# Performance work log

Hardware: AMD Instinct MI355X
Metric: run time of the kernel (lower is better)

## Reference

```python
import jax, jax.numpy as jnp
import numpy as np
from math import comb

N_DERIV = 4          # num_derivatives
ODE_DIM = 512        # ode_dimension
K = ODE_DIM * (N_DERIV + 1)


def _build_system(n, d):
    # system_matrices_1d: A_1d = flip(pascal), Q_1d = flip(hilbert), chol(Q_1d)
    x = np.arange(n + 1)
    B = np.array([[comb(i, j) for j in range(n + 1)] for i in range(n + 1)], dtype=np.float64)
    A1 = B[::-1, ::-1]                                  # flip both axes
    Hil = 1.0 / (x[:, None] + x[None, :] + 1.0)
    Q1 = Hil[::-1, ::-1]
    L1 = np.linalg.cholesky(Q1)
    a = np.kron(np.eye(d), A1)
    q = np.kron(np.eye(d), L1)
    return jnp.asarray(a, jnp.float32), jnp.asarray(q, jnp.float32)


def _qr_r(x):
    # sqrtm_to_cholesky: upper-triangular factor from reduced QR
    return jnp.linalg.qr(x)[1]


def setup_inputs() -> dict:
    key = jax.random.key(0)
    k1, k2, k3, k4, k5 = jax.random.split(key, 5)
    a, q_sqrtm_lower = _build_system(N_DERIV, ODE_DIM)
    m0 = jax.random.normal(k1, (K,), dtype=jnp.float32)
    l0 = jnp.tril(jax.random.normal(k2, (K, K), dtype=jnp.float32) * 0.05)
    H = jax.random.normal(k3, (ODE_DIM, K), dtype=jnp.float32) * 0.1
    bias = jax.random.normal(k4, (ODE_DIM,), dtype=jnp.float32)
    dt = jax.random.uniform(k5, (1,), dtype=jnp.float32, minval=0.05, maxval=0.15)
    return {"m0": m0, "l0": l0, "H": H, "bias": bias, "dt": dt,
            "a": a, "q_sqrtm_lower": q_sqrtm_lower}


def reference(m0, l0, H, bias, dt, a, q_sqrtm_lower):
    d = H.shape[0]
    k = m0.shape[0]
    n1 = k // d                       # num_derivatives + 1
    # --- assemble_preconditioner ---
    powers = jnp.arange(n1 - 1, -1, -1, dtype=m0.dtype)
    scales = jnp.exp(jax.lax.lgamma(powers + 1.0))
    pw = powers + 0.5
    adt = jnp.abs(dt[0])
    p = jnp.tile(adt ** pw / scales, d)          # (k,)
    p_inv = jnp.tile(adt ** (-pw) * scales, d)   # (k,)
    # --- extrapolate_mean ---
    m0_p = p_inv * m0
    m_ext_p = a @ m0_p
    m_ext = p * m_ext_p
    # EK-style linearized observation residual
    m_obs = H @ m_ext - bias                     # (d,)
    # --- estimate_error ---
    l_obs_ns_e = H @ (p_inv[:, None] * q_sqrtm_lower)            # (d,k)
    l_obs_raw = _qr_r(l_obs_ns_e.T).T                            # lower (d,d)
    res_white = jax.scipy.linalg.solve_triangular(l_obs_raw.T, m_obs, lower=False)
    diffusion = jnp.sqrt(jnp.dot(res_white, res_white) / res_white.size)
    error = diffusion * jnp.sqrt(jnp.einsum('nj,nj->n', l_obs_raw, l_obs_raw))
    # --- complete_extrapolation (sum_of_sqrtm_factors) ---
    R1 = (a @ (p_inv[:, None] * l0)).T           # (k,k)
    R2 = (diffusion * q_sqrtm_lower).T           # (k,k)
    l_ext_p = _qr_r(jnp.vstack([R1, R2])).T      # lower (k,k)
    l_ext = p[:, None] * l_ext_p
    # --- final_correction ---
    l_obs_ns = H @ l_ext                         # (d,k)
    l_obs = _qr_r(l_obs_ns.T).T                  # lower (d,d)
    crosscov = l_ext @ l_obs_ns.T                # (k,d)
    gain = jax.scipy.linalg.cho_solve((l_obs, True), crosscov.T).T  # (k,d)
    m_cor = m_ext - gain @ m_obs
    l_cor = l_ext - gain @ l_obs_ns
    u = jnp.reshape(m_cor, (-1, d), order='F')[0]  # derivative-0 block
    return m_cor, l_cor, u, error, diffusion
```

## Files before the change

kernel.cpp:

```cpp
#include <hip/hip_runtime.h>
#include <math.h>

#define KDIM 2560
#define DDIM 512
#define NB 64

#define QM 2560
#define QM2 1024
#define QN 512
#define PW 16
#define QACT 528

#define OUT_LCOR 2560
#define OUT_U    6556160
#define OUT_ERR  6556672
#define OUT_DIFF 6557184


__global__ void k_setup(const float* dt, double* scal){
  if (threadIdx.x==0 && blockIdx.x==0){
    double adt = fabs((double)dt[0]);
    const double scales[5] = {24.0,6.0,2.0,1.0,1.0};
    for (int i=0;i<5;i++){
      double pw = (double)(4-i)+0.5;
      scal[i]   = pow(adt, pw)/scales[i];
      scal[5+i] = pow(adt,-pw)*scales[i];
    }
  }
}

__global__ __launch_bounds__(256) void k_mext_mobs(const float* a, const float* m0, const float* H,
                                                   const float* bias, const double* scal,
                                                   double* mext, double* mobs){
  __shared__ double me[KDIM];
  __shared__ double red[256];
  double pp[5], pv[5];
  #pragma unroll
  for (int i=0;i<5;i++){ pp[i]=scal[i]; pv[i]=scal[5+i]; }
  int tid=threadIdx.x;
  for (int r=tid; r<KDIM; r+=256){
    int j=r/5, i=r%5;
    const float* arow = a + (size_t)r*KDIM + 5*j;
    const float* m0b  = m0 + 5*j;
    double acc=0;
    #pragma unroll
    for (int l=0;l<5;l++) acc += (double)arow[l]*pv[l]*(double)m0b[l];
    me[r] = pp[i]*acc;
  }
  __syncthreads();
  if (blockIdx.x==0) for (int r=tid;r<KDIM;r+=256) mext[r]=me[r];
  int b = blockIdx.x;
  const float* Hr = H + (size_t)b*KDIM;
  double acc=0;
  for (int c=tid;c<KDIM;c+=256) acc += (double)Hr[c]*me[c];
  red[tid]=acc; __syncthreads();
  for (int s=128;s>0;s>>=1){ if (tid<s) red[tid]+=red[tid+s]; __syncthreads(); }
  if (tid==0) mobs[b] = red[0] - (double)bias[b];
}

__global__ void k_A2(const float* H, const float* q, const double* scal,
                     double* Atop, double* Abot){
  int idx = blockIdx.x*blockDim.x+threadIdx.x;
  if (idx >= QN*QM) return;
  double pv[5];
  #pragma unroll
  for (int t=0;t<5;t++) pv[t]=scal[5+t];
  int j = idx / QM;
  int i = idx % QM;
  int bi = i/5;
  double acc=0;
  #pragma unroll
  for (int t=0;t<5;t++)
    acc += (double)H[(size_t)j*QM + 5*bi+t]*pv[t]*(double)q[(size_t)(5*bi+t)*QM + i];
  if (i < 512) Atop[(size_t)j*QM2 + i] = acc;
  else         Abot[(size_t)j*2048 + (i-512)] = acc;
}

__global__ void k_copyB(const double* Gbot, double* AQ){
  int idx = blockIdx.x*blockDim.x+threadIdx.x;
  if (idx >= 512*512) return;
  int c = idx/512, rr = idx%512;
  AQ[(size_t)c*QM2 + 512 + rr] = (rr<=c) ? Gbot[(size_t)c*512 + rr] : 0.0;
}

__global__ __launch_bounds__(576) void qr_step(double* A, double* vhead, double* Tbufs, int p){
  int col0 = p*PW;
  int tid=threadIdx.x, wid=tid>>6, lane=tid&63;

  if (blockIdx.x > 0){
    int pc0 = col0 - PW;
    const double* T = Tbufs + (size_t)(p-1)*PW*PW;
    int cc = col0 + PW + ((int)blockIdx.x - 1);
    int m = QM2 - pc0; if (m>QACT) m=QACT;
    __shared__ double redu[9][PW];
    __shared__ double yshu[PW];
    __shared__ double wshu[PW];
    int lr = tid;
    double a = (lr<m)? A[(size_t)cc*QM2 + pc0 + lr] : 0.0;
    double vv[PW];
    #pragma unroll
    for (int j=0;j<PW;j++){
      double vj=0.0;
      if (lr<m){
        if (lr>j)       vj=A[(size_t)(pc0+j)*QM2 + pc0 + lr];
        else if (lr==j) vj=vhead[pc0+j];
      }
      vv[j]=vj;
    }
    #pragma unroll
    for (int j=0;j<PW;j++){
      double d=vv[j]*a;
      #pragma unroll
      for (int o=32;o>0;o>>=1) d+=__shfl_down(d,o);
      if (lane==0) redu[wid][j]=d;
    }
    __syncthreads();
    if (tid<PW){
      double y=0;
      #pragma unroll
      for (int t=0;t<9;t++) y+=redu[t][tid];
      yshu[tid]=y;
    }
    __syncthreads();
    if (tid<PW){
      double s=0;
      for (int t=0;t<=tid;t++) s+=T[t*PW+tid]*yshu[t];
      wshu[tid]=s;
    }
    __syncthreads();
    if (lr<m){
      double s=0;
      #pragma unroll
      for (int j=0;j<PW;j++) s+=vv[j]*wshu[j];
      A[(size_t)cc*QM2 + pc0 + lr]=a-s;
    }
    return;
  }

  __shared__ double redw[9][PW];
  __shared__ double rednorm[9];
  __shared__ double sh[3];
  __shared__ double wsh[PW];
  __shared__ double alphas[PW], betas[PW];
  __shared__ double VtVs[PW][PW];
  __shared__ double Tsh[PW][PW];
  __shared__ double redP[9][PW*PW];
  __shared__ double ysh2[PW][PW];
  __shared__ double wsh2[PW][PW];

  int m = QM2 - col0; if (m>QACT) m=QACT;
  bool on = tid < m;
  double x[PW];

  if (p>0){
    int pc0 = col0 - PW;
    const double* T = Tbufs + (size_t)(p-1)*PW*PW;
    int mp = QM2 - pc0; if (mp>QACT) mp=QACT;
    bool gA = on;
    bool gB = (tid>=560);
    int rowA = col0 + tid;
    int kB   = tid - 560;
    double vv[PW];
    #pragma unroll
    for (int j=0;j<PW;j++){
      double vj=0.0;
      if (gA){
        if (tid + PW < mp) vj = A[(size_t)(pc0+j)*QM2 + rowA];
      } else if (gB){
        if (kB>j)       vj=A[(size_t)(pc0+j)*QM2 + pc0 + kB];
        else if (kB==j) vj=vhead[pc0+j];
      }
      vv[j]=vj;
    }
    #pragma unroll
    for (int c=0;c<PW;c++){
      double a=0.0;
      if (gA)      a = A[(size_t)(col0+c)*QM2 + rowA];
      else if (gB) a = A[(size_t)(col0+c)*QM2 + pc0 + kB];
      x[c]=a;
    }
    #pragma unroll
    for (int c=0;c<PW;c++){
      #pragma unroll
      for (int j=0;j<PW;j++){
        double d=vv[j]*x[c];
        #pragma unroll
        for (int o=32;o>0;o>>=1) d+=__shfl_down(d,o);
        if (lane==0) redP[wid][c*PW+j]=d;
      }
    }
    __syncthreads();
    if (tid<PW*PW){
      double y=0;
      #pragma unroll
      for (int t=0;t<9;t++) y+=redP[t][tid];
      ysh2[tid>>4][tid&15]=y;
    }
    __syncthreads();
    if (tid<PW*PW){
      int c=tid>>4, jj=tid&15;
      double s=0;
      for (int t=0;t<=jj;t++) s+=T[t*PW+jj]*ysh2[c][t];
      wsh2[c][jj]=s;
    }
    __syncthreads();
    #pragma unroll
    for (int c=0;c<PW;c++){
      double s=0;
      #pragma unroll
      for (int j=0;j<PW;j++) s+=vv[j]*wsh2[c][j];
      x[c]-=s;
    }
    if (gB){
      #pragma unroll
      for (int c=0;c<PW;c++) A[(size_t)(col0+c)*QM2 + pc0 + kB] = x[c];
    }
    if (!on){
      #pragma unroll
      for (int c=0;c<PW;c++) x[c]=0.0;
    }
    __syncthreads();
  } else {
    #pragma unroll
    for (int j=0;j<PW;j++)
      x[j] = on ? A[(size_t)(col0+j)*QM2 + col0 + tid] : 0.0;
  }

  #pragma unroll
  for (int j=0;j<PW;j++){
    double v0 = (tid>=j && on)? x[j] : 0.0;
    double ps = v0*v0;
    #pragma unroll
    for (int o=32;o>0;o>>=1) ps += __shfl_down(ps,o);
    if (lane==0) rednorm[wid]=ps;
    if (tid==j) sh[0]=x[j];
    __syncthreads();
    if (tid==0){
      double s0=0;
      for (int t=0;t<9;t++) s0+=rednorm[t];
      double x1=sh[0];
      double nrm=sqrt(s0);
      double alpha=(x1>=0.0)?-nrm:nrm;
      double v1=x1-alpha;
      double vtv=s0-2.0*alpha*x1+alpha*alpha;
      double b=(vtv>0.0)?2.0/vtv:0.0;
      sh[1]=v1; sh[2]=b;
      alphas[j]=alpha; betas[j]=b;
      vhead[col0+j]=v1;
    }
    __syncthreads();
    if (tid==j) x[j]=sh[1];
    double b=sh[2];
    double v=(tid>=j && on)? x[j] : 0.0;
    #pragma unroll
    for (int t=0;t<PW;t++){
      if (t==j) continue;
      double pdot=v*x[t];
      #pragma unroll
      for (int o=32;o>0;o>>=1) pdot+=__shfl_down(pdot,o);
      if (lane==0) redw[wid][t]=pdot;
    }
    __syncthreads();
    if (tid<PW && tid!=j){
      double tot=0;
      #pragma unroll
      for (int t2=0;t2<9;t2++) tot+=redw[t2][tid];
      if (tid>j) wsh[tid]=b*tot;
      else       VtVs[tid][j]=tot;
    }
    __syncthreads();
    if (v!=0.0){
      #pragma unroll
      for (int t=j+1;t<PW;t++) x[t]-=wsh[t]*v;
    }
  }
  __syncthreads();
  if (tid<PW){
    int i=tid;
    Tsh[i][i]=betas[i];
    for (int j2=i+1;j2<PW;j2++){
      double z=0;
      for (int t=i;t<j2;t++) z+=Tsh[i][t]*VtVs[t][j2];
      Tsh[i][j2]=-betas[j2]*z;
    }
  }
  __syncthreads();
  for (int e=tid;e<PW*PW;e+=576){
    int i=e/PW, j2=e%PW;
    Tbufs[(size_t)p*PW*PW + e] = (j2>=i)? Tsh[i][j2] : 0.0;
  }
  if (on){
    #pragma unroll
    for (int j=0;j<PW;j++)
      A[(size_t)(col0+j)*QM2 + col0 + tid] = (tid==j)? alphas[j] : x[j];
  }
}

__global__ __launch_bounds__(512) void k_rpost(const double* Aq, const double* mobs,
                                               double* scal, float* out){
  __shared__ double b[DDIM];
  __shared__ double xs[DDIM];
  __shared__ double D[NB][NB+1];
  __shared__ double red[DDIM];
  __shared__ double g1sh[DDIM];
  int tid=threadIdx.x;
  {
    double s=0;
    for (int r=0;r<=tid;r++){ double v=Aq[(size_t)tid*QM2 + r]; s+=v*v; }
    g1sh[tid]=s;
  }
  b[tid]=mobs[tid];
  __syncthreads();
  for (int p=7;p>=0;p--){
    int b0=p*NB;
    for (int e=tid;e<NB*NB;e+=512){ int i=e&63, j2=e>>6; D[i][j2]=Aq[(size_t)(b0+j2)*QM2 + b0+i]; }
    __syncthreads();
    if (tid<64){
      double bi=b[b0+tid];
      for (int k=NB-1;k>=0;k--){
        double bk=__shfl(bi,k);
        double xk=bk/D[k][k];
        if (tid<k) bi-=D[tid][k]*xk;
        if (tid==k) bi=xk;
      }
      xs[b0+tid]=bi;
    }
    __syncthreads();
    if (tid<b0){
      double s=0;
      #pragma unroll 8
      for (int j2=0;j2<NB;j2++) s+=Aq[(size_t)(b0+j2)*QM2 + tid]*xs[b0+j2];
      b[tid]-=s;
    }
    __syncthreads();
  }
  red[tid]=xs[tid]*xs[tid]; __syncthreads();
  for (int s=256;s>0;s>>=1){ if (tid<s) red[tid]+=red[tid+s]; __syncthreads(); }
  double diff=sqrt(red[0]/(double)DDIM);
  if (tid==0){ scal[10]=diff; out[OUT_DIFF]=(float)diff; }
  out[OUT_ERR+tid]=(float)(diff*sqrt(fmax(g1sh[tid],0.0)));
}

__global__ void k_X(const float* a, const float* l0, const double* scal, float* X){
  int idx=blockIdx.x*blockDim.x+threadIdx.x;
  if (idx>=KDIM*KDIM) return;
  double pv[5];
  #pragma unroll
  for (int t=0;t<5;t++) pv[t]=scal[5+t];
  int r=idx/KDIM, c=idx%KDIM;
  int j=r/5;
  const float* arow = a + (size_t)r*KDIM + 5*j;
  double acc=0;
  #pragma unroll
  for (int l=0;l<5;l++)
    acc += (double)arow[l]*pv[l]*(double)l0[(size_t)(5*j+l)*KDIM+c];
  X[idx]=(float)acc;
}

template<typename TA,int ATR,typename TB,int BTR,int MODE>
__global__ __launch_bounds__(256) void gemm32(const TA* __restrict__ A,int lda,
                                              const TB* __restrict__ B,int ldb,
                                              void* __restrict__ Cv,int ldc,
                                              int K,int kmode){
  __shared__ double As[32][33];
  __shared__ double Bs[32][33];
  int tid=threadIdx.x, tx=tid&15, ty=tid>>4;
  int n0=blockIdx.x*32, m0=blockIdx.y*32;
  int ks=0, ke=K;
  if (kmode==1) ks=n0;
  else if (kmode==2) ke=min(K,n0+32);
  else if (kmode==3) ke=min(K,m0+32);
  else if (kmode==4) ks=m0;
  double acc[2][2]={};
  for (int k0=ks;k0<ke;k0+=32){
    if (ATR){
      for (int e=tid;e<32*32;e+=256){int k=e>>5,mm=e&31; As[k][mm]=(double)A[(size_t)(k0+k)*lda+m0+mm];}
    } else {
      for (int e=tid;e<32*32;e+=256){int mm=e>>5,k=e&31; As[k][mm]=(double)A[(size_t)(m0+mm)*lda+k0+k];}
    }
    if (BTR){
      for (int e=tid;e<32*32;e+=256){int nn=e>>5,k=e&31; Bs[k][nn]=(double)B[(size_t)(n0+nn)*ldb+k0+k];}
    } else {
      for (int e=tid;e<32*32;e+=256){int k=e>>5,nn=e&31; Bs[k][nn]=(double)B[(size_t)(k0+k)*ldb+n0+nn];}
    }
    __syncthreads();
    #pragma unroll
    for (int t=0;t<32;t++){
      double av[2],bv[2];
      #pragma unroll
      for (int i=0;i<2;i++){av[i]=As[t][ty+16*i];bv[i]=Bs[t][tx+16*i];}
      #pragma unroll
      for (int i=0;i<2;i++)
        #pragma unroll
        for (int j=0;j<2;j++) acc[i][j]+=av[i]*bv[j];
    }
    __syncthreads();
  }
  #pragma unroll
  for (int i=0;i<2;i++){
    #pragma unroll
    for (int j=0;j<2;j++){
      size_t idx=(size_t)(m0+ty+16*i)*ldc+n0+tx+16*j;
      if (MODE==0) ((double*)Cv)[idx]=acc[i][j];
      else if (MODE==1) ((double*)Cv)[idx]-=acc[i][j];
      else ((float*)Cv)[idx]=(float)acc[i][j];
    }
  }
}

__global__ __launch_bounds__(256) void syrk_lower(const float* __restrict__ X, const float* __restrict__ q,
                                                  const double* __restrict__ scal,
                                                  double* __restrict__ G, int n){
  int t = blockIdx.x;
  int u = (int)((sqrtf(8.0f*(float)t+1.0f)+1.0f)*0.5f);
  while ((u*(u-1))/2 > t) u--;
  while ((u*(u+1))/2 <= t) u++;
  int s = (KDIM/64) - u;
  int r = s + (t - (u*(u-1))/2);
  int S0=s*64, R0=r*64;
  __shared__ double As[16][65];
  __shared__ double Bs[16][65];
  int tid=threadIdx.x, tx=tid&15, ty=tid>>4;
  int kend=min(n, S0+80);
  double acc[4][4]={};
  for (int k0=0;k0<kend;k0+=16){
    for (int e=tid;e<64*16;e+=256){int mm=e>>4,k=e&15; As[k][mm]=(double)X[(size_t)(R0+mm)*n+k0+k];}
    for (int e=tid;e<64*16;e+=256){int nn=e>>4,k=e&15; Bs[k][nn]=(double)X[(size_t)(S0+nn)*n+k0+k];}
    __syncthreads();
    #pragma unroll
    for (int t2=0;t2<16;t2++){
      double av[4],bv[4];
      #pragma unroll
      for (int i=0;i<4;i++){av[i]=As[t2][ty+16*i];bv[i]=Bs[t2][tx+16*i];}
      #pragma unroll
      for (int i=0;i<4;i++)
        #pragma unroll
        for (int j=0;j<4;j++) acc[i][j]+=av[i]*bv[j];
    }
    __syncthreads();
  }
  double dd = scal[10]*scal[10];
  #pragma unroll
  for (int i=0;i<4;i++)
    #pragma unroll
    for (int j=0;j<4;j++){
      int rr=R0+ty+16*i, c=S0+tx+16*j;
      double v=acc[i][j];
      if (c<=rr && (rr/5)==(c/5)){
        double qq=0;
        #pragma unroll
        for (int k=0;k<5;k++) qq += (double)q[(size_t)(rr%5)*KDIM+k]*(double)q[(size_t)(c%5)*KDIM+k];
        v += dd*qq;
      }
      G[(size_t)rr*n+c]=v;
    }
}

__global__ __launch_bounds__(256) void chol_diag(double* A, int n, int k0){
  __shared__ double P[NB][NB+1];
  int tid=threadIdx.x;
  for (int e=tid;e<NB*NB;e+=256){int r=e>>6,c=e&63;P[r][c]=A[(size_t)(k0+r)*n+k0+c];}
  int tx=tid&15, ty=tid>>4;
  __syncthreads();
  for (int j=0;j<NB;j++){
    double pj=P[j][j];
    __syncthreads();
    double rpj=1.0/sqrt(fmax(pj,1e-280));
    if (tid>j && tid<NB) P[tid][j]*=rpj;
    if (tid==j) P[j][j]=sqrt(fmax(pj,1e-280));
    __syncthreads();
    #pragma unroll
    for (int a2=0;a2<4;a2++){
      int r=ty+16*a2;
      double lrj=P[r][j];
      #pragma unroll
      for (int b2=0;b2<4;b2++){
        int c=tx+16*b2;
        if (r>j && c>j && c<=r) P[r][c]-=lrj*P[c][j];
      }
    }
    __syncthreads();
  }
  for (int e=tid;e<NB*NB;e+=256){int r=e>>6,c=e&63;A[(size_t)(k0+r)*n+k0+c]=P[r][c];}
}

__global__ __launch_bounds__(256) void chol_step(double* __restrict__ A, int n, int k0){
  __shared__ double Ls[NB][NB+1];
  __shared__ double rec[NB];
  __shared__ double As[16][65];
  __shared__ double Bs[16][65];
  int ts0=k0+NB;
  int t=blockIdx.x;
  int r=(int)((sqrtf(8.0f*(float)t+1.0f)-1.0f)*0.5f);
  while ((r*(r+1))/2 > t) r--;
  while (((r+1)*(r+2))/2 <= t) r++;
  int s=t-(r*(r+1))/2;
  int R0=ts0+r*NB, S0=ts0+s*NB;
  int tid=threadIdx.x, tx=tid&15, ty=tid>>4;
  for (int e=tid;e<NB*NB;e+=256){int rr=e>>6,c=e&63;Ls[rr][c]=A[(size_t)(k0+rr)*n+k0+c];}
  __syncthreads();
  if (tid<NB) rec[tid]=1.0/Ls[tid][tid];
  __syncthreads();
  double ar[NB];
  bool solver = (tid<64) || (tid<128 && s!=r);
  int srow = (tid<64)? (R0+tid) : (S0+(tid-64));
  if (solver){
    #pragma unroll
    for (int c=0;c<NB;c++) ar[c]=A[(size_t)srow*n + k0 + c];
    #pragma unroll
    for (int j=0;j<NB;j++){
      double sv=ar[j];
      #pragma unroll
      for (int t2=0;t2<j;t2++) sv-=ar[t2]*Ls[j][t2];
      ar[j]=sv*rec[j];
    }
  }
  double acc[4][4]={};
  #pragma unroll
  for (int c4=0;c4<4;c4++){
    __syncthreads();
    if (tid<64){
      #pragma unroll
      for (int k=0;k<16;k++) As[k][tid]=ar[c4*16+k];
      if (s==r){
        #pragma unroll
        for (int k=0;k<16;k++) Bs[k][tid]=ar[c4*16+k];
      }
    } else if (tid<128 && s!=r){
      #pragma unroll
      for (int k=0;k<16;k++) Bs[k][tid-64]=ar[c4*16+k];
    }
    __syncthreads();
    #pragma unroll
    for (int tt=0;tt<16;tt++){
      double av[4],bv[4];
      #pragma unroll
      for (int i=0;i<4;i++){av[i]=As[tt][ty+16*i];bv[i]=Bs[tt][tx+16*i];}
      #pragma unroll
      for (int i=0;i<4;i++)
        #pragma unroll
        for (int j=0;j<4;j++) acc[i][j]+=av[i]*bv[j];
    }
  }
  __syncthreads();
  if (t!=0){
    #pragma unroll
    for (int i=0;i<4;i++)
      #pragma unroll
      for (int j=0;j<4;j++)
        A[(size_t)(R0+ty+16*i)*n+S0+tx+16*j]-=acc[i][j];
    return;
  }
  double (*P)[NB+1] = Ls;
  #pragma unroll
  for (int i=0;i<4;i++)
    #pragma unroll
    for (int j=0;j<4;j++)
      P[ty+16*i][tx+16*j] = A[(size_t)(ts0+ty+16*i)*n+ts0+tx+16*j] - acc[i][j];
  __syncthreads();
  for (int j=0;j<NB;j++){
    double pj=P[j][j];
    __syncthreads();
    double rpj=1.0/sqrt(fmax(pj,1e-280));
    if (tid>j && tid<NB) P[tid][j]*=rpj;
    if (tid==j) P[j][j]=sqrt(fmax(pj,1e-280));
    __syncthreads();
    #pragma unroll
    for (int a2=0;a2<4;a2++){
      int r2=ty+16*a2;
      double lrj=P[r2][j];
      #pragma unroll
      for (int b2=0;b2<4;b2++){
        int c=tx+16*b2;
        if (r2>j && c>j && c<=r2) P[r2][c]-=lrj*P[c][j];
      }
    }
    __syncthreads();
  }
  for (int e=tid;e<NB*NB;e+=256){int r2=e>>6,c=e&63;A[(size_t)(ts0+r2)*n+ts0+c]=P[r2][c];}
}

__global__ __launch_bounds__(256) void chol_sweep(double* A, int n){
  __shared__ double Ls[NB][NB+1];
  __shared__ double St[NB][NB+1];
  __shared__ double rec[NB];
  int k0=blockIdx.y*NB;
  int base=k0+NB+blockIdx.x*256;
  if (base>=n) return;
  int tid=threadIdx.x;
  for (int e=tid;e<NB*NB;e+=256){int r2=e>>6,c=e&63;Ls[r2][c]=A[(size_t)(k0+r2)*n+k0+c];}
  __syncthreads();
  if (tid<NB) rec[tid]=1.0/Ls[tid][tid];
  int myrow=base+tid, mychunk=tid>>6, lrow=tid&63;
  double ar[NB];
  for (int ch=0;ch<4;ch++){
    int r0=base+ch*64;
    for (int e=tid;e<NB*NB;e+=256){
      int r2=e>>6,c=e&63;
      if (r0+r2<n) St[r2][c]=A[(size_t)(r0+r2)*n+k0+c];
    }
    __syncthreads();
    if (mychunk==ch && myrow<n){
      #pragma unroll
      for (int c=0;c<NB;c++) ar[c]=St[lrow][c];
    }
    __syncthreads();
  }
  if (myrow<n){
    #pragma unroll
    for (int j=0;j<NB;j++){
      double s2=ar[j];
      #pragma unroll
      for (int t2=0;t2<j;t2++) s2-=ar[t2]*Ls[j][t2];
      ar[j]=s2*rec[j];
    }
  }
  for (int ch=0;ch<4;ch++){
    int r0=base+ch*64;
    if (mychunk==ch && myrow<n){
      #pragma unroll
      for (int c=0;c<NB;c++) St[lrow][c]=ar[c];
    }
    __syncthreads();
    for (int e=tid;e<NB*NB;e+=256){
      int r2=e>>6,c=e&63;
      if (r0+r2<n) A[(size_t)(r0+r2)*n+k0+c]=St[r2][c];
    }
    __syncthreads();
  }
}

__global__ void k_extract(const double* G2, const double* scal, float* lext){
  int idx=blockIdx.x*blockDim.x+threadIdx.x;
  if (idx>=KDIM*KDIM) return;
  int r=idx/KDIM, c=idx%KDIM;
  double v = (c<=r)? scal[r%5]*G2[idx] : 0.0;
  lext[idx]=(float)v;
}

__global__ __launch_bounds__(256) void trinv_diag(const double* S, double* Linv){
  __shared__ double Ls[NB][NB+1];
  __shared__ double Ti[NB][NB+1];
  int jb=blockIdx.x, tid=threadIdx.x;
  for (int e=tid; e<DDIM*NB; e+=256){
    int r=e/NB, c=e%NB;
    Linv[(size_t)r*DDIM + jb*NB + c]=0.0;
  }
  for (int e=tid;e<NB*NB;e+=256){int r=e>>6,c=e&63; Ls[r][c]=S[(size_t)(jb*NB+r)*DDIM + jb*NB+c];}
  __syncthreads();
  if (tid<NB){
    int c=tid;
    for (int r=c;r<NB;r++){
      double s=(r==c)?1.0:0.0;
      for (int t=c;t<r;t++) s-=Ls[r][t]*Ti[t][c];
      Ti[r][c]=s/Ls[r][r];
    }
    for (int r=0;r<c;r++) Ti[r][c]=0.0;
  }
  __syncthreads();
  for (int e=tid;e<NB*NB;e+=256){int r=e>>6,c=e&63; Linv[(size_t)(jb*NB+r)*DDIM + jb*NB+c]=Ti[r][c];}
}

__global__ __launch_bounds__(256) void trinv_step(const double* S, double* Linv, int d){
  __shared__ double As[16][65];
  __shared__ double Bs[16][65];
  __shared__ double Ps[NB][NB+1];
  int jb=blockIdx.x, ib=jb+d;
  int tid=threadIdx.x, tx=tid&15, ty=tid>>4;
  double acc[4][4]={};
  int kstart=jb*NB, kend=ib*NB;
  for (int k0=kstart;k0<kend;k0+=16){
    for (int e=tid;e<64*16;e+=256){int mm=e>>4,k=e&15; As[k][mm]=S[(size_t)(ib*NB+mm)*DDIM + k0+k];}
    for (int e=tid;e<16*64;e+=256){int k=e>>6,nn=e&63; Bs[k][nn]=Linv[(size_t)(k0+k)*DDIM + jb*NB+nn];}
    __syncthreads();
    #pragma unroll
    for (int t=0;t<16;t++){
      double av[4],bv[4];
      #pragma unroll
      for (int i=0;i<4;i++){av[i]=As[t][ty+16*i];bv[i]=Bs[t][tx+16*i];}
      #pragma unroll
      for (int i=0;i<4;i++)
        #pragma unroll
        for (int j=0;j<4;j++) acc[i][j]+=av[i]*bv[j];
    }
    __syncthreads();
  }
  #pragma unroll
  for (int i=0;i<4;i++)
    #pragma unroll
    for (int j=0;j<4;j++) Ps[ty+16*i][tx+16*j]=acc[i][j];
  double o[4][4]={};
  __syncthreads();
  for (int k0=0;k0<NB;k0+=16){
    for (int e=tid;e<64*16;e+=256){int mm=e>>4,k=e&15; As[k][mm]=Linv[(size_t)(ib*NB+mm)*DDIM + ib*NB+k0+k];}
    __syncthreads();
    #pragma unroll
    for (int t=0;t<16;t++){
      double av[4],bv[4];
      #pragma unroll
      for (int i=0;i<4;i++){av[i]=As[t][ty+16*i];bv[i]=Ps[k0+t][tx+16*i];}
      #pragma unroll
      for (int i=0;i<4;i++)
        #pragma unroll
        for (int j=0;j<4;j++) o[i][j]+=av[i]*bv[j];
    }
    __syncthreads();
  }
  #pragma unroll
  for (int i=0;i<4;i++)
    #pragma unroll
    for (int j=0;j<4;j++)
      Linv[(size_t)(ib*NB+ty+16*i)*DDIM + jb*NB+tx+16*j] = -o[i][j];
}

__global__ void k_mcor(const double* Z, const double* mobs, const double* mext, float* out){
  __shared__ double mo[DDIM];
  for (int s=threadIdx.x;s<DDIM;s+=256) mo[s]=mobs[s];
  __syncthreads();
  int r=blockIdx.x*256+threadIdx.x;
  if (r>=KDIM) return;
  double acc=0;
  for (int s=0;s<DDIM;s++) acc += Z[(size_t)s*KDIM+r]*mo[s];
  double mc = mext[r]-acc;
  out[r]=(float)mc;
  if (r%5==0) out[OUT_U + r/5]=(float)mc;
}

__global__ __launch_bounds__(256) void k_lcor(const double* __restrict__ Z, const float* __restrict__ lobs,
                                              const float* __restrict__ lext, float* __restrict__ out){
  __shared__ double As[16][65];
  __shared__ double Bs[16][65];
  int tid=threadIdx.x, tx=tid&15, ty=tid>>4;
  int n0=blockIdx.x*64, m0=blockIdx.y*64;
  double acc[4][4]={};
  for (int k0=0;k0<DDIM;k0+=16){
    for (int e=tid;e<16*64;e+=256){int k=e>>6,mm=e&63; As[k][mm]=Z[(size_t)(k0+k)*KDIM+m0+mm];}
    for (int e=tid;e<16*64;e+=256){int k=e>>6,nn=e&63; Bs[k][nn]=(double)lobs[(size_t)(k0+k)*KDIM+n0+nn];}
    __syncthreads();
    #pragma unroll
    for (int t=0;t<16;t++){
      double av[4],bv[4];
      #pragma unroll
      for (int i=0;i<4;i++){av[i]=As[t][ty+16*i];bv[i]=Bs[t][tx+16*i];}
      #pragma unroll
      for (int i=0;i<4;i++)
        #pragma unroll
        for (int j=0;j<4;j++) acc[i][j]+=av[i]*bv[j];
    }
    __syncthreads();
  }
  #pragma unroll
  for (int i=0;i<4;i++)
    #pragma unroll
    for (int j=0;j<4;j++){
      size_t idx=(size_t)(m0+ty+16*i)*KDIM+n0+tx+16*j;
      out[OUT_LCOR+idx]=(float)((double)lext[idx]-acc[i][j]);
    }
}

extern "C" void kernel_launch(void* const* d_in, const int* in_sizes, int n_in,
                              void* d_out, int out_size, void* d_ws, size_t ws_size,
                              hipStream_t stream) {
  const float* m0  = (const float*)d_in[0];
  const float* l0  = (const float*)d_in[1];
  const float* H   = (const float*)d_in[2];
  const float* bias= (const float*)d_in[3];
  const float* dt  = (const float*)d_in[4];
  const float* a   = (const float*)d_in[5];
  const float* q   = (const float*)d_in[6];
  float* out = (float*)d_out;

  char* w=(char*)d_ws;
  auto alloc=[&](size_t bytes)->char*{ char* p=w; w += ((bytes+255)/256)*256; return p; };
  double* scal  =(double*)alloc(16*8);
  double* mext  =(double*)alloc((size_t)KDIM*8);
  double* mobs  =(double*)alloc((size_t)DDIM*8);
  double* vheadA=(double*)alloc((size_t)QN*8);
  double* Tbufs =(double*)alloc((size_t)(QN/PW)*PW*PW*8);
  double* AQ    =(double*)alloc((size_t)QM2*QN*8);
  double* S     =(double*)alloc((size_t)DDIM*DDIM*8);
  double* G2    =(double*)alloc((size_t)KDIM*KDIM*8);
  float*  LOBS  =(float*) alloc((size_t)DDIM*KDIM*4);
  float*  X     =(float*) alloc((size_t)KDIM*KDIM*4);
  float*  LEXT  = X;
  double* Abot  = G2;
  double* Gbot  = Abot + (size_t)2048*512;
  double* Linv  = G2;
  double* C2    = Linv + (size_t)DDIM*DDIM;
  double* Y     = C2   + (size_t)DDIM*KDIM;
  double* Z     = Y    + (size_t)DDIM*KDIM;

  auto chol_full=[&](double* M, int n){
    chol_diag<<<1,256,0,stream>>>(M, n, 0);
    for (int k0=0;k0+NB<n;k0+=NB){
      int T = (n-k0-NB)/NB;
      chol_step<<<T*(T+1)/2,256,0,stream>>>(M,n,k0);
    }
    dim3 g((n-NB+255)/256, n/NB-1);
    chol_sweep<<<g,256,0,stream>>>(M,n);
  };

  k_setup<<<1,1,0,stream>>>(dt, scal);
  k_mext_mobs<<<DDIM,256,0,stream>>>(a, m0, H, bias, scal, mext, mobs);

  k_A2<<<(QN*QM+255)/256,256,0,stream>>>(H, q, scal, AQ, Abot);
  gemm32<double,0,double,1,0><<<dim3(16,16),256,0,stream>>>(Abot,2048, Abot,2048, Gbot,512, 2048, 0);
  chol_full(Gbot, 512);
  k_copyB<<<(512*512+255)/256,256,0,stream>>>(Gbot, AQ);
  for (int p=0;p<QN/PW;p++){
    int nlz = QN - (p+1)*PW;
    int grid = 1 + ((p>0)? nlz : 0);
    qr_step<<<grid,576,0,stream>>>(AQ, vheadA, Tbufs, p);
  }
  k_rpost<<<1,512,0,stream>>>(AQ, mobs, scal, out);

  k_X<<<(KDIM*KDIM+255)/256,256,0,stream>>>(a, l0, scal, X);
  syrk_lower<<<(KDIM/64)*((KDIM/64)+1)/2,256,0,stream>>>(X, q, scal, G2, KDIM);
  chol_full(G2, KDIM);
  k_extract<<<(KDIM*KDIM+255)/256,256,0,stream>>>(G2, scal, LEXT);

  gemm32<float,0,float,0,2><<<dim3(KDIM/32,DDIM/32),256,0,stream>>>(H,KDIM, LEXT,KDIM, LOBS,KDIM, KDIM, 1);
  gemm32<float,0,float,1,0><<<dim3(DDIM/32,DDIM/32),256,0,stream>>>(LOBS,KDIM, LOBS,KDIM, S,DDIM, KDIM, 0);
  chol_full(S, DDIM);
  trinv_diag<<<8,256,0,stream>>>(S, Linv);
  for (int d=1;d<8;d++)
    trinv_step<<<8-d,256,0,stream>>>(S, Linv, d);
  gemm32<float,0,float,1,0><<<dim3(KDIM/32,DDIM/32),256,0,stream>>>(LOBS,KDIM, LEXT,KDIM, C2,KDIM, KDIM, 2);
  gemm32<double,0,double,0,0><<<dim3(KDIM/32,DDIM/32),256,0,stream>>>(Linv,DDIM, C2,KDIM, Y,KDIM, DDIM, 3);
  gemm32<double,1,double,0,0><<<dim3(KDIM/32,DDIM/32),256,0,stream>>>(Linv,DDIM, Y,KDIM, Z,KDIM, DDIM, 4);

  k_mcor<<<(KDIM+255)/256,256,0,stream>>>(Z, mobs, mext, out);
  k_lcor<<<dim3(KDIM/64,KDIM/64),256,0,stream>>>(Z, LOBS, LEXT, out);
}
```

Measured before the change: 15.00 ms.

## Replace full triangular inverse with blocked forward/back cho_solve fused with mcor

Drops the seven trinv_step launches and the two dense Linv GEMMs, and adds one cho_solve kernel. For each 64-column slab it runs a blocked forward and backward substitution against the Cholesky factor, using only the inverted diagonal blocks, then computes m_cor inside the same kernel. The syrk and lcor tile loads now read float4 vectors instead of scalars. The solve runs on only 40 blocks and walks its 8 block-rows in sequence, so it has little parallelism and may be latency-bound.

```diff
diff --git a/kernel.cpp b/kernel.cpp
--- a/kernel.cpp
+++ b/kernel.cpp
@@ -423,9 +423,16 @@
   int tid=threadIdx.x, tx=tid&15, ty=tid>>4;
   int kend=min(n, S0+80);
   double acc[4][4]={};
+  int mm=tid>>2, f=tid&3;
   for (int k0=0;k0<kend;k0+=16){
-    for (int e=tid;e<64*16;e+=256){int mm=e>>4,k=e&15; As[k][mm]=(double)X[(size_t)(R0+mm)*n+k0+k];}
-    for (int e=tid;e<64*16;e+=256){int nn=e>>4,k=e&15; Bs[k][nn]=(double)X[(size_t)(S0+nn)*n+k0+k];}
+    {
+      float4 xa = *(const float4*)(X + (size_t)(R0+mm)*n + k0 + 4*f);
+      float4 xb = *(const float4*)(X + (size_t)(S0+mm)*n + k0 + 4*f);
+      As[4*f+0][mm]=(double)xa.x; As[4*f+1][mm]=(double)xa.y;
+      As[4*f+2][mm]=(double)xa.z; As[4*f+3][mm]=(double)xa.w;
+      Bs[4*f+0][mm]=(double)xb.x; Bs[4*f+1][mm]=(double)xb.y;
+      Bs[4*f+2][mm]=(double)xb.z; Bs[4*f+3][mm]=(double)xb.w;
+    }
     __syncthreads();
     #pragma unroll
     for (int t2=0;t2<16;t2++){
@@ -642,10 +649,6 @@
   __shared__ double Ls[NB][NB+1];
   __shared__ double Ti[NB][NB+1];
   int jb=blockIdx.x, tid=threadIdx.x;
-  for (int e=tid; e<DDIM*NB; e+=256){
-    int r=e/NB, c=e%NB;
-    Linv[(size_t)r*DDIM + jb*NB + c]=0.0;
-  }
   for (int e=tid;e<NB*NB;e+=256){int r=e>>6,c=e&63; Ls[r][c]=S[(size_t)(jb*NB+r)*DDIM + jb*NB+c];}
   __syncthreads();
   if (tid<NB){
@@ -661,69 +664,144 @@
   for (int e=tid;e<NB*NB;e+=256){int r=e>>6,c=e&63; Linv[(size_t)(jb*NB+r)*DDIM + jb*NB+c]=Ti[r][c];}
 }
 
-__global__ __launch_bounds__(256) void trinv_step(const double* S, double* Linv, int d){
-  __shared__ double As[16][65];
-  __shared__ double Bs[16][65];
-  __shared__ double Ps[NB][NB+1];
-  int jb=blockIdx.x, ib=jb+d;
+__global__ __launch_bounds__(256) void cho_solve(const double* __restrict__ Lm,
+                                                 const double* __restrict__ Li,
+                                                 const double* __restrict__ B,
+                                                 double* __restrict__ Zt,
+                                                 const double* __restrict__ mobs,
+                                                 const double* __restrict__ mext,
+                                                 float* __restrict__ out){
+  __shared__ double Ld[16][65];
+  __shared__ double Ws[NB][NB+1];
+  int cb = blockIdx.x*NB;
   int tid=threadIdx.x, tx=tid&15, ty=tid>>4;
-  double acc[4][4]={};
-  int kstart=jb*NB, kend=ib*NB;
-  for (int k0=kstart;k0<kend;k0+=16){
-    for (int e=tid;e<64*16;e+=256){int mm=e>>4,k=e&15; As[k][mm]=S[(size_t)(ib*NB+mm)*DDIM + k0+k];}
-    for (int e=tid;e<16*64;e+=256){int k=e>>6,nn=e&63; Bs[k][nn]=Linv[(size_t)(k0+k)*DDIM + jb*NB+nn];}
-    __syncthreads();
-    #pragma unroll
-    for (int t=0;t<16;t++){
-      double av[4],bv[4];
-      #pragma unroll
-      for (int i=0;i<4;i++){av[i]=As[t][ty+16*i];bv[i]=Bs[t][tx+16*i];}
-      #pragma unroll
-      for (int i=0;i<4;i++)
-        #pragma unroll
-        for (int j=0;j<4;j++) acc[i][j]+=av[i]*bv[j];
-    }
-    __syncthreads();
-  }
-  #pragma unroll
-  for (int i=0;i<4;i++)
-    #pragma unroll
-    for (int j=0;j<4;j++) Ps[ty+16*i][tx+16*j]=acc[i][j];
-  double o[4][4]={};
-  __syncthreads();
-  for (int k0=0;k0<NB;k0+=16){
-    for (int e=tid;e<64*16;e+=256){int mm=e>>4,k=e&15; As[k][mm]=Linv[(size_t)(ib*NB+mm)*DDIM + ib*NB+k0+k];}
-    __syncthreads();
-    #pragma unroll
-    for (int t=0;t<16;t++){
-      double av[4],bv[4];
-      #pragma unroll
-      for (int i=0;i<4;i++){av[i]=As[t][ty+16*i];bv[i]=Ps[k0+t][tx+16*i];}
-      #pragma unroll
-      for (int i=0;i<4;i++)
-        #pragma unroll
-        for (int j=0;j<4;j++) o[i][j]+=av[i]*bv[j];
-    }
-    __syncthreads();
-  }
-  #pragma unroll
-  for (int i=0;i<4;i++)
-    #pragma unroll
-    for (int j=0;j<4;j++)
-      Linv[(size_t)(ib*NB+ty+16*i)*DDIM + jb*NB+tx+16*j] = -o[i][j];
-}
-
-__global__ void k_mcor(const double* Z, const double* mobs, const double* mext, float* out){
-  __shared__ double mo[DDIM];
-  for (int s=threadIdx.x;s<DDIM;s+=256) mo[s]=mobs[s];
-  __syncthreads();
-  int r=blockIdx.x*256+threadIdx.x;
-  if (r>=KDIM) return;
-  double acc=0;
-  for (int s=0;s<DDIM;s++) acc += Z[(size_t)s*KDIM+r]*mo[s];
-  double mc = mext[r]-acc;
-  out[r]=(float)mc;
-  if (r%5==0) out[OUT_U + r/5]=(float)mc;
+
+  for (int p=0;p<8;p++){
+    double acc[4][4];
+    #pragma unroll
+    for (int i=0;i<4;i++)
+      #pragma unroll
+      for (int j=0;j<4;j++)
+        acc[i][j]=B[(size_t)(p*NB+ty+16*i)*KDIM + cb+tx+16*j];
+    for (int q=0;q<p;q++){
+      __syncthreads();
+      for (int e=tid;e<NB*NB;e+=256){int rr=e>>6,c=e&63; Ws[rr][c]=Zt[(size_t)(q*NB+rr)*KDIM + cb+c];}
+      #pragma unroll
+      for (int c4=0;c4<4;c4++){
+        __syncthreads();
+        for (int e=tid;e<16*NB;e+=256){int rr=e&63,k=e>>6; Ld[k][rr]=Lm[(size_t)(p*NB+rr)*DDIM + q*NB+c4*16+k];}
+        __syncthreads();
+        #pragma unroll
+        for (int k=0;k<16;k++){
+          double av[4],bv[4];
+          #pragma unroll
+          for (int i=0;i<4;i++){av[i]=Ld[k][ty+16*i]; bv[i]=Ws[c4*16+k][tx+16*i];}
+          #pragma unroll
+          for (int i=0;i<4;i++)
+            #pragma unroll
+            for (int j=0;j<4;j++) acc[i][j]-=av[i]*bv[j];
+        }
+      }
+    }
+    __syncthreads();
+    #pragma unroll
+    for (int i=0;i<4;i++)
+      #pragma unroll
+      for (int j=0;j<4;j++) Ws[ty+16*i][tx+16*j]=acc[i][j];
+    double xr[4][4]={};
+    #pragma unroll
+    for (int c4=0;c4<4;c4++){
+      __syncthreads();
+      for (int e=tid;e<16*NB;e+=256){int rr=e&63,k=e>>6; Ld[k][rr]=Li[(size_t)(p*NB+rr)*DDIM + p*NB+c4*16+k];}
+      __syncthreads();
+      #pragma unroll
+      for (int k=0;k<16;k++){
+        double av[4],bv[4];
+        #pragma unroll
+        for (int i=0;i<4;i++){av[i]=Ld[k][ty+16*i]; bv[i]=Ws[c4*16+k][tx+16*i];}
+        #pragma unroll
+        for (int i=0;i<4;i++)
+          #pragma unroll
+          for (int j=0;j<4;j++) xr[i][j]+=av[i]*bv[j];
+      }
+    }
+    #pragma unroll
+    for (int i=0;i<4;i++)
+      #pragma unroll
+      for (int j=0;j<4;j++)
+        Zt[(size_t)(p*NB+ty+16*i)*KDIM + cb+tx+16*j]=xr[i][j];
+    __syncthreads();
+  }
+  for (int p=7;p>=0;p--){
+    double acc[4][4];
+    #pragma unroll
+    for (int i=0;i<4;i++)
+      #pragma unroll
+      for (int j=0;j<4;j++)
+        acc[i][j]=Zt[(size_t)(p*NB+ty+16*i)*KDIM + cb+tx+16*j];
+    for (int q=p+1;q<8;q++){
+      __syncthreads();
+      for (int e=tid;e<NB*NB;e+=256){int rr=e>>6,c=e&63; Ws[rr][c]=Zt[(size_t)(q*NB+rr)*KDIM + cb+c];}
+      #pragma unroll
+      for (int c4=0;c4<4;c4++){
+        __syncthreads();
+        for (int e=tid;e<16*NB;e+=256){int rr=e&63,k=e>>6; Ld[k][rr]=Lm[(size_t)(q*NB+c4*16+k)*DDIM + p*NB+rr];}
+        __syncthreads();
+        #pragma unroll
+        for (int k=0;k<16;k++){
+          double av[4],bv[4];
+          #pragma unroll
+          for (int i=0;i<4;i++){av[i]=Ld[k][ty+16*i]; bv[i]=Ws[c4*16+k][tx+16*i];}
+          #pragma unroll
+          for (int i=0;i<4;i++)
+            #pragma unroll
+            for (int j=0;j<4;j++) acc[i][j]-=av[i]*bv[j];
+        }
+      }
+    }
+    __syncthreads();
+    #pragma unroll
+    for (int i=0;i<4;i++)
+      #pragma unroll
+      for (int j=0;j<4;j++) Ws[ty+16*i][tx+16*j]=acc[i][j];
+    double xr[4][4]={};
+    #pragma unroll
+    for (int c4=0;c4<4;c4++){
+      __syncthreads();
+      for (int e=tid;e<16*NB;e+=256){int rr=e&63,k=e>>6; Ld[k][rr]=Li[(size_t)(p*NB+c4*16+k)*DDIM + p*NB+rr];}
+      __syncthreads();
+      #pragma unroll
+      for (int k=0;k<16;k++){
+        double av[4],bv[4];
+        #pragma unroll
+        for (int i=0;i<4;i++){av[i]=Ld[k][ty+16*i]; bv[i]=Ws[c4*16+k][tx+16*i];}
+        #pragma unroll
+        for (int i=0;i<4;i++)
+          #pragma unroll
+          for (int j=0;j<4;j++) xr[i][j]+=av[i]*bv[j];
+      }
+    }
+    #pragma unroll
+    for (int i=0;i<4;i++)
+      #pragma unroll
+      for (int j=0;j<4;j++)
+        Zt[(size_t)(p*NB+ty+16*i)*KDIM + cb+tx+16*j]=xr[i][j];
+    __syncthreads();
+  }
+  {
+    int c=tid&63, qu=tid>>6;
+    double s=0;
+    for (int s0=qu*128; s0<qu*128+128; s0++)
+      s += Zt[(size_t)s0*KDIM + cb + c]*mobs[s0];
+    __syncthreads();
+    Ws[qu][c]=s;
+    __syncthreads();
+    if (tid<64){
+      double mc = mext[cb+tid] - (Ws[0][tid]+Ws[1][tid]+Ws[2][tid]+Ws[3][tid]);
+      out[cb+tid]=(float)mc;
+      if ((cb+tid)%5==0) out[OUT_U+(cb+tid)/5]=(float)mc;
+    }
+  }
 }
 
 __global__ __launch_bounds__(256) void k_lcor(const double* __restrict__ Z, const float* __restrict__ lobs,
@@ -733,9 +811,14 @@
   int tid=threadIdx.x, tx=tid&15, ty=tid>>4;
   int n0=blockIdx.x*64, m0=blockIdx.y*64;
   double acc[4][4]={};
+  int kk=tid>>4, f=tid&15;
   for (int k0=0;k0<DDIM;k0+=16){
     for (int e=tid;e<16*64;e+=256){int k=e>>6,mm=e&63; As[k][mm]=Z[(size_t)(k0+k)*KDIM+m0+mm];}
-    for (int e=tid;e<16*64;e+=256){int k=e>>6,nn=e&63; Bs[k][nn]=(double)lobs[(size_t)(k0+k)*KDIM+n0+nn];}
+    {
+      float4 xb = *(const float4*)(lobs + (size_t)(k0+kk)*KDIM + n0 + 4*f);
+      Bs[kk][4*f+0]=(double)xb.x; Bs[kk][4*f+1]=(double)xb.y;
+      Bs[kk][4*f+2]=(double)xb.z; Bs[kk][4*f+3]=(double)xb.w;
+    }
     __syncthreads();
     #pragma unroll
     for (int t=0;t<16;t++){
@@ -823,12 +906,7 @@
   gemm32<float,0,float,1,0><<<dim3(DDIM/32,DDIM/32),256,0,stream>>>(LOBS,KDIM, LOBS,KDIM, S,DDIM, KDIM, 0);
   chol_full(S, DDIM);
   trinv_diag<<<8,256,0,stream>>>(S, Linv);
-  for (int d=1;d<8;d++)
-    trinv_step<<<8-d,256,0,stream>>>(S, Linv, d);
   gemm32<float,0,float,1,0><<<dim3(KDIM/32,DDIM/32),256,0,stream>>>(LOBS,KDIM, LEXT,KDIM, C2,KDIM, KDIM, 2);
-  gemm32<double,0,double,0,0><<<dim3(KDIM/32,DDIM/32),256,0,stream>>>(Linv,DDIM, C2,KDIM, Y,KDIM, DDIM, 3);
-  gemm32<double,1,double,0,0><<<dim3(KDIM/32,DDIM/32),256,0,stream>>>(Linv,DDIM, Y,KDIM, Z,KDIM, DDIM, 4);
-
-  k_mcor<<<(KDIM+255)/256,256,0,stream>>>(Z, mobs, mext, out);
+  cho_solve<<<KDIM/NB,256,0,stream>>>(S, Linv, C2, Z, mobs, mext, out);
   k_lcor<<<dim3(KDIM/64,KDIM/64),256,0,stream>>>(Z, LOBS, LEXT, out);
 }
```

Measured after the change: 16.33 ms. 1.09x slower.
